# Kernel tuning notes

Hardware: AMD Instinct MI355X
Metric: run time of the kernel (lower is better)

The kernel has to match this reference:

```python
import jax, jax.numpy as jnp
import numpy as np

LATENT = 256


def setup_inputs() -> dict:
    key = jax.random.key(0)
    ks = jax.random.split(key, 10)
    B, T, V, E, D0, H, L = 512, 200, 3356, 1128, 20000, 1024, LATENT

    def glorot(k, shape):
        fan_out, fan_in = shape
        std = np.sqrt(2.0 / (fan_in + fan_out)).astype(np.float32)
        return jax.random.normal(k, shape, dtype=jnp.float32) * std

    x = jax.random.uniform(ks[0], (B, D0), dtype=jnp.float32)
    item_ids = jax.random.randint(ks[1], (B, T), 0, V, dtype=jnp.int32)
    embed = jax.random.normal(ks[2], (V, E), dtype=jnp.float32)
    Wi = glorot(ks[3], (L, E))
    bi = jnp.zeros((L,), jnp.float32)
    We1 = glorot(ks[4], (H, D0))
    be1 = jnp.zeros((H,), jnp.float32)
    We2 = glorot(ks[5], (2 * L, H))
    be2 = jnp.zeros((2 * L,), jnp.float32)
    Wd1 = glorot(ks[6], (H, L))
    bd1 = jnp.zeros((H,), jnp.float32)
    Wd2 = glorot(ks[7], (D0, H))
    bd2 = jnp.zeros((D0,), jnp.float32)
    # dropout(p=0.5) mask, pre-scaled by 1/(1-p)=2
    drop_mask = (jax.random.bernoulli(ks[8], 0.5, (B, D0))).astype(jnp.float32) * 2.0
    eps = jax.random.normal(ks[9], (B, L), dtype=jnp.float32)
    return {"x": x, "item_ids": item_ids, "embed": embed, "Wi": Wi, "bi": bi,
            "We1": We1, "be1": be1, "We2": We2, "be2": be2,
            "Wd1": Wd1, "bd1": bd1, "Wd2": Wd2, "bd2": bd2,
            "drop_mask": drop_mask, "eps": eps}


def reference(x, item_ids, embed, Wi, bi, We1, be1, We2, be2,
              Wd1, bd1, Wd2, bd2, drop_mask, eps):
    # item feature path: embedding lookup -> linear -> per-sequence stats
    item = jnp.einsum('bte,le->btl', embed[item_ids], Wi) + bi        # [B,T,L]
    mean = jnp.mean(item, axis=1)                                      # [B,L]
    deviation = jnp.std(item, axis=1, ddof=1)                          # torch.std (unbiased)

    # encoder: F.normalize (L2 over features) -> dropout -> tanh MLP
    xn = x / jnp.maximum(jnp.linalg.norm(x, axis=1, keepdims=True), 1e-12)
    h = xn * drop_mask
    h = jnp.tanh(h @ We1.T + be1)
    gparams = h @ We2.T + be2                                          # [B,2L]
    mu, logvar = gparams[:, :LATENT], gparams[:, LATENT:]

    # reparam: MVN with diagonal covariance diag(deviation) == mean + sqrt(dev)*eps
    prior = mean + jnp.sqrt(deviation) * eps
    z = prior * jnp.exp(0.5 * logvar) + mu

    # decoder: tanh MLP
    hd = jnp.tanh(z @ Wd1.T + bd1)
    recon_x = hd @ Wd2.T + bd2                                         # [B,D0]
    return recon_x, mu, logvar
```

## Files before the change

### kernel.cpp

```cpp
#include <hip/hip_runtime.h>
#include <hip/hip_bf16.h>

typedef __bf16 bf16x8 __attribute__((ext_vector_type(8)));
typedef float f32x4 __attribute__((ext_vector_type(4)));
typedef unsigned short u16x8 __attribute__((ext_vector_type(8)));

static __device__ __forceinline__ unsigned short f2bf(float f){
  unsigned int u = __float_as_uint(f);
  u += 0x7fffu + ((u >> 16) & 1u);
  return (unsigned short)(u >> 16);
}

static __device__ __forceinline__ u16x8 cvt8(const float4& a, const float4& b){
  u16x8 r;
  r[0]=f2bf(a.x); r[1]=f2bf(a.y); r[2]=f2bf(a.z); r[3]=f2bf(a.w);
  r[4]=f2bf(b.x); r[5]=f2bf(b.y); r[6]=f2bf(b.z); r[7]=f2bf(b.w);
  return r;
}

static __device__ __forceinline__ void gload16(const void* g, void* l){
  __builtin_amdgcn_global_load_lds(
      (const __attribute__((address_space(1))) unsigned int*)g,
      (__attribute__((address_space(3))) unsigned int*)l, 16, 0, 0);
}

template<int EPI>
__global__ __launch_bounds__(256) void gemm_bf(
    const unsigned short* __restrict__ A, const unsigned short* __restrict__ Bw,
    const float* __restrict__ bias,
    float* __restrict__ Cf, unsigned short* __restrict__ Cbf,
    int M, int N, int K, int kchunk)
{
  constexpr int BM = 128, BN = 128, BK = 32;
  __shared__ unsigned short lds[(BM + BN) * BK];
  unsigned short* lA = lds;
  unsigned short* lB = lds + BM * BK;

  const int tid  = threadIdx.x, lane = tid & 63, wave = tid >> 6;
  const int bm0  = blockIdx.y * BM, bn0 = blockIdx.x * BN;
  const int k0   = blockIdx.z * kchunk;
  const int kend = min(K, k0 + kchunk);
  const int fr = lane & 15, fq = lane >> 4;
  const int wm = (wave >> 1) * 64, wn = (wave & 1) * 64;

  const bool isA  = wave < 2;
  const int cbase = (wave & 1) * 4;
  const int srow  = lane >> 2, scol = (lane & 3) * 8;
  const unsigned short* G = isA ? A : Bw;
  const int glim = (isA ? M : N) - 1;
  const int g0   = isA ? bm0 : bn0;
  unsigned short* ldst = isA ? lA : lB;

  f32x4 acc[4][4] = {};

  for (int kk = k0; kk < kend; kk += BK) {
    #pragma unroll
    for (int c = 0; c < 4; c++) {
      const int ch = cbase + c;
      const int r = min(g0 + ch * 16 + srow, glim);
      gload16(G + (size_t)r * K + kk + scol, (char*)ldst + ch * 1024);
    }
    __syncthreads();
    u16x8 af[4], bg[4];
    #pragma unroll
    for (int i = 0; i < 4; i++) af[i] = *(const u16x8*)&lA[(wm + i*16 + fr) * BK + fq * 8];
    #pragma unroll
    for (int j = 0; j < 4; j++) bg[j] = *(const u16x8*)&lB[(wn + j*16 + fr) * BK + fq * 8];
    #pragma unroll
    for (int i = 0; i < 4; i++)
      #pragma unroll
      for (int j = 0; j < 4; j++)
        acc[i][j] = __builtin_amdgcn_mfma_f32_16x16x32_bf16(
            __builtin_bit_cast(bf16x8, af[i]),
            __builtin_bit_cast(bf16x8, bg[j]),
            acc[i][j], 0, 0, 0);
    __syncthreads();
  }

  #pragma unroll
  for (int i = 0; i < 4; i++)
    #pragma unroll
    for (int j = 0; j < 4; j++)
      #pragma unroll
      for (int r = 0; r < 4; r++) {
        int row = bm0 + wm + i*16 + fq*4 + r;
        int col = bn0 + wn + j*16 + fr;
        if (row < M && col < N) {
          float v = acc[i][j][r];
          if constexpr (EPI == 0) {
            Cf[(size_t)row * N + col] = v + (bias ? bias[col] : 0.0f);
          } else if constexpr (EPI == 1) {
            atomicAdd(&Cf[(size_t)row * N + col], v);
          } else {
            Cbf[(size_t)row * N + col] = f2bf(tanhf(v + bias[col]));
          }
        }
      }
}

__global__ __launch_bounds__(256) void cvt4_kernel(
    const float* __restrict__ s0, unsigned short* __restrict__ d0, int n0,
    const float* __restrict__ s1, unsigned short* __restrict__ d1, int n1,
    const float* __restrict__ s2, unsigned short* __restrict__ d2, int n2,
    const float* __restrict__ s3, unsigned short* __restrict__ d3, int n3)
{
  int i = (blockIdx.x * 256 + threadIdx.x) * 8;
  const float* s; unsigned short* d;
  if (i < n0)            { s = s0; d = d0; }
  else if ((i -= n0) < n1) { s = s1; d = d1; }
  else if ((i -= n1) < n2) { s = s2; d = d2; }
  else if ((i -= n2) < n3) { s = s3; d = d3; }
  else return;
  const float4* q = (const float4*)(s + i);
  *(u16x8*)(d + i) = cvt8(q[0], q[1]);
}

__global__ __launch_bounds__(256) void cvtpad_kernel(
    const float* __restrict__ src, unsigned short* __restrict__ dst,
    int rows, int scols, int dcols)
{
  int i8 = blockIdx.x * 256 + threadIdx.x;
  int c8 = dcols / 8;
  if (i8 >= rows * c8) return;
  int r = i8 / c8, c0 = (i8 % c8) * 8;
  const float* s = src + (size_t)r * scols;
  u16x8 o;
  #pragma unroll
  for (int e = 0; e < 8; e++) { int c = c0 + e; o[e] = (c < scols) ? f2bf(s[c]) : (unsigned short)0; }
  *(u16x8*)(dst + (size_t)r * dcols + c0) = o;
}

__global__ __launch_bounds__(256) void ynorm_kernel(
    const float* __restrict__ x, const float* __restrict__ dm,
    unsigned short* __restrict__ y, float* __restrict__ ninv, int D0)
{
  const int b = blockIdx.x, tid = threadIdx.x;
  const float4* x4 = (const float4*)(x + (size_t)b * D0);
  const float4* d4 = (const float4*)(dm + (size_t)b * D0);
  ushort4* y4 = (ushort4*)(y + (size_t)b * D0);
  const int n4 = D0 / 4;
  float ss = 0.f;
  for (int i = tid; i < n4; i += 256) {
    float4 xv = x4[i], dv = d4[i];
    ss += xv.x*xv.x + xv.y*xv.y + xv.z*xv.z + xv.w*xv.w;
    ushort4 o;
    o.x = f2bf(xv.x*dv.x); o.y = f2bf(xv.y*dv.y);
    o.z = f2bf(xv.z*dv.z); o.w = f2bf(xv.w*dv.w);
    y4[i] = o;
  }
  #pragma unroll
  for (int off = 32; off > 0; off >>= 1) ss += __shfl_down(ss, off);
  __shared__ float wsum[4];
  if ((tid & 63) == 0) wsum[tid >> 6] = ss;
  __syncthreads();
  if (tid == 0) {
    float t = wsum[0] + wsum[1] + wsum[2] + wsum[3];
    ninv[b] = 1.0f / fmaxf(sqrtf(t), 1e-12f);
  }
}

__global__ __launch_bounds__(256) void stats_kernel(
    const float* __restrict__ proj, const int* __restrict__ ids,
    const float* __restrict__ bi, const float* __restrict__ eps,
    float* __restrict__ prior, int T)
{
  const int b = blockIdx.x, l = threadIdx.x;
  __shared__ int sid[256];
  if (l < T) sid[l] = ids[b * T + l];
  __syncthreads();
  float s1 = 0.f, s2 = 0.f;
  #pragma unroll 4
  for (int t = 0; t < T; t++) {
    float p = proj[(size_t)sid[t] * 256 + l];
    s1 += p; s2 += p * p;
  }
  float var = fmaxf((s2 - s1 * s1 / (float)T) / (float)(T - 1), 0.f);
  float dev = sqrtf(var);
  float mean = s1 / (float)T + bi[l];
  prior[b * 256 + l] = mean + sqrtf(dev) * eps[b * 256 + l];
}

__global__ __launch_bounds__(256) void epi1_kernel(
    const float* __restrict__ C1, const float* __restrict__ ninv,
    const float* __restrict__ be1, unsigned short* __restrict__ h)
{
  int i = blockIdx.x * 256 + threadIdx.x;
  int b = i >> 10, n = i & 1023;
  h[i] = f2bf(tanhf(ninv[b] * C1[i] + be1[n]));
}

__global__ __launch_bounds__(256) void z_kernel(
    const float* __restrict__ gp, const float* __restrict__ prior,
    const float* __restrict__ be2,
    float* __restrict__ out_mu, float* __restrict__ out_lv,
    unsigned short* __restrict__ z)
{
  int i = blockIdx.x * 256 + threadIdx.x;
  int b = i >> 8, l = i & 255;
  float mu = gp[b * 512 + l]       + be2[l];
  float lv = gp[b * 512 + 256 + l] + be2[256 + l];
  out_mu[i] = mu;
  out_lv[i] = lv;
  z[i] = f2bf(prior[i] * expf(0.5f * lv) + mu);
}

extern "C" void kernel_launch(void* const* d_in, const int* in_sizes, int n_in,
                              void* d_out, int out_size, void* d_ws, size_t ws_size,
                              hipStream_t stream)
{
  const float* x     = (const float*)d_in[0];
  const int*   ids   = (const int*)  d_in[1];
  const float* embed = (const float*)d_in[2];
  const float* Wi    = (const float*)d_in[3];
  const float* bi    = (const float*)d_in[4];
  const float* We1   = (const float*)d_in[5];
  const float* be1   = (const float*)d_in[6];
  const float* We2   = (const float*)d_in[7];
  const float* be2   = (const float*)d_in[8];
  const float* Wd1   = (const float*)d_in[9];
  const float* bd1   = (const float*)d_in[10];
  const float* Wd2   = (const float*)d_in[11];
  const float* bd2   = (const float*)d_in[12];
  const float* dm    = (const float*)d_in[13];
  const float* eps   = (const float*)d_in[14];

  constexpr int B = 512, T = 200, V = 3356, E = 1128, Ep = 1152, D0 = 20000, H = 1024, L = 256;

  char* w = (char*)d_ws;
  auto carve = [&](size_t bytes) { char* p = w; w += (bytes + 255) & ~(size_t)255; return p; };
  unsigned short* We1b  = (unsigned short*)carve((size_t)H * D0 * 2);
  unsigned short* Wd2b  = (unsigned short*)carve((size_t)D0 * H * 2);
  unsigned short* We2b  = (unsigned short*)carve((size_t)2 * L * H * 2);
  unsigned short* Wd1b  = (unsigned short*)carve((size_t)H * L * 2);
  unsigned short* embedb= (unsigned short*)carve((size_t)V * Ep * 2);
  unsigned short* Wib   = (unsigned short*)carve((size_t)L * Ep * 2);
  float*          proj  = (float*)         carve((size_t)V * L * 4);
  unsigned short* y     = (unsigned short*)carve((size_t)B * D0 * 2);
  float*          C1    = (float*)         carve((size_t)B * H * 4);
  unsigned short* h     = (unsigned short*)carve((size_t)B * H * 2);
  float*          gp    = (float*)         carve((size_t)B * 2 * L * 4);
  float*          prior = (float*)         carve((size_t)B * L * 4);
  unsigned short* z     = (unsigned short*)carve((size_t)B * L * 2);
  unsigned short* hd    = (unsigned short*)carve((size_t)B * H * 2);
  float*          ninv  = (float*)         carve((size_t)B * 4);

  float* out_recon = (float*)d_out;
  float* out_mu    = out_recon + (size_t)B * D0;
  float* out_lv    = out_mu + (size_t)B * L;

  {
    const int n0 = H * D0, n1 = D0 * H, n2 = 2 * L * H, n3 = H * L;
    const int nblk = (n0 + n1 + n2 + n3) / (8 * 256);
    cvt4_kernel<<<nblk, 256, 0, stream>>>(We1, We1b, n0, Wd2, Wd2b, n1,
                                          We2, We2b, n2, Wd1, Wd1b, n3);
  }
  cvtpad_kernel<<<(V * (Ep/8) + 255) / 256, 256, 0, stream>>>(embed, embedb, V, E, Ep);
  cvtpad_kernel<<<(L * (Ep/8) + 255) / 256, 256, 0, stream>>>(Wi, Wib, L, E, Ep);

  ynorm_kernel<<<B, 256, 0, stream>>>(x, dm, y, ninv, D0);

  hipMemsetAsync(proj, 0, (size_t)V * L * 4, stream);
  gemm_bf<1><<<dim3(2, 27, 4), 256, 0, stream>>>(
      embedb, Wib, nullptr, proj, nullptr, V, L, Ep, 288);
  stats_kernel<<<B, 256, 0, stream>>>(proj, ids, bi, eps, prior, T);

  hipMemsetAsync(C1, 0, (size_t)B * H * 4, stream);
  gemm_bf<1><<<dim3(8, 4, 25), 256, 0, stream>>>(
      y, We1b, nullptr, C1, nullptr, B, H, D0, 800);
  epi1_kernel<<<(B * H) / 256, 256, 0, stream>>>(C1, ninv, be1, h);

  hipMemsetAsync(gp, 0, (size_t)B * 2 * L * 4, stream);
  gemm_bf<1><<<dim3(4, 4, 4), 256, 0, stream>>>(
      h, We2b, nullptr, gp, nullptr, B, 2 * L, H, 256);
  z_kernel<<<(B * L) / 256, 256, 0, stream>>>(gp, prior, be2, out_mu, out_lv, z);

  gemm_bf<2><<<dim3(8, 4, 1), 256, 0, stream>>>(
      z, Wd1b, bd1, nullptr, hd, B, H, L, 256);
  gemm_bf<0><<<dim3(157, 4, 1), 256, 0, stream>>>(
      hd, Wd2b, bd2, out_recon, nullptr, B, D0, H, 1024);
}
```

Before: 313.1 us.

## Fuse fp32-to-bf16 weight conversion into GEMM loads with double-buffered pipeline

Drops the standalone weight conversion kernels and instead has each GEMM load fp32 weight tiles into registers, convert them to bf16, and store them into LDS. The GEMM main loop is also restructured into a two-stage double-buffered pipeline with prefetch of the next tiles issued before the MFMAs. This removes a full read-and-write pass over roughly 40M weight elements. In exchange the GEMMs read twice as many weight bytes and do conversion work per tile, which may be repeated across M-blocks.

Result: slower. 365.3 us (+16.7%).

```diff
diff --git a/kernel.cpp b/kernel.cpp
--- a/kernel.cpp
+++ b/kernel.cpp
@@ -11,10 +11,10 @@
   return (unsigned short)(u >> 16);
 }
 
-static __device__ __forceinline__ u16x8 cvt8(const float4& a, const float4& b){
+static __device__ __forceinline__ u16x8 cvt8(const f32x4& a, const f32x4& b){
   u16x8 r;
-  r[0]=f2bf(a.x); r[1]=f2bf(a.y); r[2]=f2bf(a.z); r[3]=f2bf(a.w);
-  r[4]=f2bf(b.x); r[5]=f2bf(b.y); r[6]=f2bf(b.z); r[7]=f2bf(b.w);
+  r[0]=f2bf(a[0]); r[1]=f2bf(a[1]); r[2]=f2bf(a[2]); r[3]=f2bf(a[3]);
+  r[4]=f2bf(b[0]); r[5]=f2bf(b[1]); r[6]=f2bf(b[2]); r[7]=f2bf(b[3]);
   return r;
 }
 
@@ -25,47 +25,83 @@
 }
 
 template<int EPI>
-__global__ __launch_bounds__(256) void gemm_bf(
-    const unsigned short* __restrict__ A, const unsigned short* __restrict__ Bw,
+__global__ __launch_bounds__(256) void gemm_mx(
+    const unsigned short* __restrict__ A, const float* __restrict__ Bw,
     const float* __restrict__ bias,
     float* __restrict__ Cf, unsigned short* __restrict__ Cbf,
-    int M, int N, int K, int kchunk)
-{
-  constexpr int BM = 128, BN = 128, BK = 32;
-  __shared__ unsigned short lds[(BM + BN) * BK];
-  unsigned short* lA = lds;
-  unsigned short* lB = lds + BM * BK;
+    int M, int N, int KA, int KB, int kchunk)
+{
+  constexpr int BK = 32, BUFE = 8192;
+  __shared__ unsigned short lds[2 * BUFE];
 
   const int tid  = threadIdx.x, lane = tid & 63, wave = tid >> 6;
-  const int bm0  = blockIdx.y * BM, bn0 = blockIdx.x * BN;
+  const int bm0  = blockIdx.y * 128, bn0 = blockIdx.x * 128;
   const int k0   = blockIdx.z * kchunk;
-  const int kend = min(K, k0 + kchunk);
+  const int kend = min(KA, k0 + kchunk);
+  const int nk   = (kend - k0) / BK;
   const int fr = lane & 15, fq = lane >> 4;
   const int wm = (wave >> 1) * 64, wn = (wave & 1) * 64;
 
-  const bool isA  = wave < 2;
-  const int cbase = (wave & 1) * 4;
-  const int srow  = lane >> 2, scol = (lane & 3) * 8;
-  const unsigned short* G = isA ? A : Bw;
-  const int glim = (isA ? M : N) - 1;
-  const int g0   = isA ? bm0 : bn0;
-  unsigned short* ldst = isA ? lA : lB;
+  const int arow0 = bm0 + wave * 32 + (lane >> 2);
+  const int acol  = (lane & 3) * 8;
+  const int brow = min(bn0 + (tid >> 1), N - 1);
+  const int bcol = (tid & 1) * 16;
+  const float* Brow = Bw + (size_t)brow * KB;
+
+  auto stageA = [&](int buf, int t){
+    unsigned short* dst = lds + buf * BUFE;
+    const int kk = k0 + t * BK;
+    #pragma unroll
+    for (int c = 0; c < 2; c++) {
+      const int r = min(arow0 + c * 16, M - 1);
+      gload16(A + (size_t)r * KA + kk + acol,
+              (char*)dst + wave * 2048 + c * 1024);
+    }
+  };
+  auto loadB = [&](int t, f32x4 (&rb)[4]){
+    const int kk = k0 + t * BK + bcol;
+    #pragma unroll
+    for (int q = 0; q < 4; q++) {
+      const int c = kk + q * 4;
+      const f32x4 v = *(const f32x4*)(Brow + min(c, KB - 4));
+      const f32x4 z4 = {0.f,0.f,0.f,0.f};
+      rb[q] = (c < KB) ? v : z4;
+    }
+  };
+  auto writeB = [&](int buf, const f32x4 (&rb)[4]){
+    unsigned short* d = lds + buf * BUFE + 4096 + (tid >> 1) * 32 + (tid & 1) * 16;
+    *(u16x8*)(d)     = cvt8(rb[0], rb[1]);
+    *(u16x8*)(d + 8) = cvt8(rb[2], rb[3]);
+  };
+
+  f32x4 rb0[4], rb1[4];
+  stageA(0, 0); loadB(0, rb0);
+  if (nk > 1) { stageA(1, 1); loadB(1, rb1); }
 
   f32x4 acc[4][4] = {};
-
-  for (int kk = k0; kk < kend; kk += BK) {
-    #pragma unroll
-    for (int c = 0; c < 4; c++) {
-      const int ch = cbase + c;
-      const int r = min(g0 + ch * 16 + srow, glim);
-      gload16(G + (size_t)r * K + kk + scol, (char*)ldst + ch * 1024);
-    }
-    __syncthreads();
+  int t = 0;
+
+  auto iter = [&](f32x4 (&rb)[4]){
+    if (t < nk - 1) asm volatile("s_waitcnt vmcnt(6)" ::: "memory");
+    else            asm volatile("s_waitcnt vmcnt(0)" ::: "memory");
+    writeB(t & 1, rb);
+    asm volatile("s_waitcnt lgkmcnt(0)" ::: "memory");
+    __builtin_amdgcn_sched_barrier(0);
+    __builtin_amdgcn_s_barrier();
+
+    const unsigned short* lA = lds + (t & 1) * BUFE;
+    const unsigned short* lB = lA + 4096;
     u16x8 af[4], bg[4];
     #pragma unroll
     for (int i = 0; i < 4; i++) af[i] = *(const u16x8*)&lA[(wm + i*16 + fr) * BK + fq * 8];
     #pragma unroll
     for (int j = 0; j < 4; j++) bg[j] = *(const u16x8*)&lB[(wn + j*16 + fr) * BK + fq * 8];
+    asm volatile("s_waitcnt lgkmcnt(0)" ::: "memory");
+    __builtin_amdgcn_sched_barrier(0);
+    __builtin_amdgcn_s_barrier();
+
+    if (t + 2 < nk) { stageA(t & 1, t + 2); loadB(t + 2, rb); }
+
     #pragma unroll
     for (int i = 0; i < 4; i++)
       #pragma unroll
@@ -74,8 +110,11 @@
             __builtin_bit_cast(bf16x8, af[i]),
             __builtin_bit_cast(bf16x8, bg[j]),
             acc[i][j], 0, 0, 0);
-    __syncthreads();
-  }
+    ++t;
+  };
+
+  while (t + 1 < nk) { iter(rb0); iter(rb1); }
+  if (t < nk) iter(rb0);
 
   #pragma unroll
   for (int i = 0; i < 4; i++)
@@ -96,23 +135,6 @@
           }
         }
       }
-}
-
-__global__ __launch_bounds__(256) void cvt4_kernel(
-    const float* __restrict__ s0, unsigned short* __restrict__ d0, int n0,
-    const float* __restrict__ s1, unsigned short* __restrict__ d1, int n1,
-    const float* __restrict__ s2, unsigned short* __restrict__ d2, int n2,
-    const float* __restrict__ s3, unsigned short* __restrict__ d3, int n3)
-{
-  int i = (blockIdx.x * 256 + threadIdx.x) * 8;
-  const float* s; unsigned short* d;
-  if (i < n0)            { s = s0; d = d0; }
-  else if ((i -= n0) < n1) { s = s1; d = d1; }
-  else if ((i -= n1) < n2) { s = s2; d = d2; }
-  else if ((i -= n2) < n3) { s = s3; d = d3; }
-  else return;
-  const float4* q = (const float4*)(s + i);
-  *(u16x8*)(d + i) = cvt8(q[0], q[1]);
 }
 
 __global__ __launch_bounds__(256) void cvtpad_kernel(
@@ -228,12 +250,7 @@
 
   char* w = (char*)d_ws;
   auto carve = [&](size_t bytes) { char* p = w; w += (bytes + 255) & ~(size_t)255; return p; };
-  unsigned short* We1b  = (unsigned short*)carve((size_t)H * D0 * 2);
-  unsigned short* Wd2b  = (unsigned short*)carve((size_t)D0 * H * 2);
-  unsigned short* We2b  = (unsigned short*)carve((size_t)2 * L * H * 2);
-  unsigned short* Wd1b  = (unsigned short*)carve((size_t)H * L * 2);
   unsigned short* embedb= (unsigned short*)carve((size_t)V * Ep * 2);
-  unsigned short* Wib   = (unsigned short*)carve((size_t)L * Ep * 2);
   float*          proj  = (float*)         carve((size_t)V * L * 4);
   unsigned short* y     = (unsigned short*)carve((size_t)B * D0 * 2);
   float*          C1    = (float*)         carve((size_t)B * H * 4);
@@ -248,34 +265,27 @@
   float* out_mu    = out_recon + (size_t)B * D0;
   float* out_lv    = out_mu + (size_t)B * L;
 
-  {
-    const int n0 = H * D0, n1 = D0 * H, n2 = 2 * L * H, n3 = H * L;
-    const int nblk = (n0 + n1 + n2 + n3) / (8 * 256);
-    cvt4_kernel<<<nblk, 256, 0, stream>>>(We1, We1b, n0, Wd2, Wd2b, n1,
-                                          We2, We2b, n2, Wd1, Wd1b, n3);
-  }
   cvtpad_kernel<<<(V * (Ep/8) + 255) / 256, 256, 0, stream>>>(embed, embedb, V, E, Ep);
-  cvtpad_kernel<<<(L * (Ep/8) + 255) / 256, 256, 0, stream>>>(Wi, Wib, L, E, Ep);
 
   ynorm_kernel<<<B, 256, 0, stream>>>(x, dm, y, ninv, D0);
 
   hipMemsetAsync(proj, 0, (size_t)V * L * 4, stream);
-  gemm_bf<1><<<dim3(2, 27, 4), 256, 0, stream>>>(
-      embedb, Wib, nullptr, proj, nullptr, V, L, Ep, 288);
+  gemm_mx<1><<<dim3(2, 27, 4), 256, 0, stream>>>(
+      embedb, Wi, nullptr, proj, nullptr, V, L, Ep, E, 288);
   stats_kernel<<<B, 256, 0, stream>>>(proj, ids, bi, eps, prior, T);
 
   hipMemsetAsync(C1, 0, (size_t)B * H * 4, stream);
-  gemm_bf<1><<<dim3(8, 4, 25), 256, 0, stream>>>(
-      y, We1b, nullptr, C1, nullptr, B, H, D0, 800);
+  gemm_mx<1><<<dim3(8, 4, 25), 256, 0, stream>>>(
+      y, We1, nullptr, C1, nullptr, B, H, D0, D0, 800);
   epi1_kernel<<<(B * H) / 256, 256, 0, stream>>>(C1, ninv, be1, h);
 
   hipMemsetAsync(gp, 0, (size_t)B * 2 * L * 4, stream);
-  gemm_bf<1><<<dim3(4, 4, 4), 256, 0, stream>>>(
-      h, We2b, nullptr, gp, nullptr, B, 2 * L, H, 256);
+  gemm_mx<1><<<dim3(4, 4, 4), 256, 0, stream>>>(
+      h, We2, nullptr, gp, nullptr, B, 2 * L, H, H, 256);
   z_kernel<<<(B * L) / 256, 256, 0, stream>>>(gp, prior, be2, out_mu, out_lv, z);
 
-  gemm_bf<2><<<dim3(8, 4, 1), 256, 0, stream>>>(
-      z, Wd1b, bd1, nullptr, hd, B, H, L, 256);
-  gemm_bf<0><<<dim3(157, 4, 1), 256, 0, stream>>>(
-      hd, Wd2b, bd2, out_recon, nullptr, B, D0, H, 1024);
-}
+  gemm_mx<2><<<dim3(8, 4, 1), 256, 0, stream>>>(
+      z, Wd1, bd1, nullptr, hd, B, H, L, L, 256);
+  gemm_mx<0><<<dim3(157, 4, 1), 256, 0, stream>>>(
+      hd, Wd2, bd2, out_recon, nullptr, B, D0, H, H, 1024);
+}
```
